# Kernel tuning notes

Measured on AMD Instinct MI355X. Metric: run time of the kernel, lower is better.

## Reference

```python
import jax, jax.numpy as jnp
import numpy as np

B, S, D = 8, 1024, 1024
N_HEAD, N_ACTIVE, D_ATTN = 16, 4, 128

def setup_inputs() -> dict:
    key = jax.random.key(0)
    ks = jax.random.split(key, 8)
    sc = 0.02
    return {
        "x": jax.random.normal(ks[0], (B, S, D), jnp.float32),
        "Wq": jax.random.normal(ks[1], (N_HEAD, D, D_ATTN), jnp.float32) * sc,
        "bq": jnp.zeros((N_HEAD, D_ATTN), jnp.float32),
        "Wk": jax.random.normal(ks[2], (N_HEAD, D, D_ATTN), jnp.float32) * sc,
        "bk": jnp.zeros((N_HEAD, D_ATTN), jnp.float32),
        "Wv": jax.random.normal(ks[3], (N_HEAD, D, D_ATTN), jnp.float32) * sc,
        "bv": jnp.zeros((N_HEAD, D_ATTN), jnp.float32),
        "Wr": jax.random.normal(ks[4], (D, N_HEAD), jnp.float32) * sc,
        "br": jnp.zeros((N_HEAD,), jnp.float32),
        "Wo": jax.random.normal(ks[5], (N_ACTIVE * D_ATTN, D), jnp.float32) * sc,
        "bo": jnp.zeros((D,), jnp.float32),
    }

def reference(x, Wq, bq, Wk, bk, Wv, bv, Wr, br, Wo, bo):
    # ---- routing: mean-pool router logits over seq, softmax over heads ----
    logits = jnp.einsum('bsd,dh->bsh', x, Wr) + br          # [B,S,H]
    dist = jax.nn.softmax(logits.mean(axis=1), axis=-1)     # [B,H]
    vals, idx = jax.lax.top_k(dist, N_ACTIVE)               # [B,A]
    # zeros + scatter of top-k probs, then softmax over ALL heads (as in source)
    sparse = jnp.zeros_like(dist).at[jnp.arange(B)[:, None], idx].set(vals)
    gates_full = jax.nn.softmax(sparse, axis=-1)            # [B,H]
    gates = jnp.take_along_axis(gates_full, idx, axis=-1)   # [B,A]
    # ---- gather active-head projection weights per batch ----
    Wq_a, Wk_a, Wv_a = Wq[idx], Wk[idx], Wv[idx]            # [B,A,D,Dk]
    bq_a, bk_a, bv_a = bq[idx], bk[idx], bv[idx]            # [B,A,Dk]
    Q = jnp.einsum('bsd,badk->bask', x, Wq_a) + bq_a[:, :, None, :]
    K = jnp.einsum('bsd,badk->bask', x, Wk_a) + bk_a[:, :, None, :]
    V = jnp.einsum('bsd,badk->bask', x, Wv_a) + bv_a[:, :, None, :]
    scale = 1.0 / jnp.sqrt(jnp.asarray(D_ATTN, x.dtype))
    scores = jax.nn.softmax(jnp.einsum('bask,batk->bast', Q, K) * scale, axis=-1)
    heads = jnp.einsum('bast,batk->bask', scores, V)        # [B,A,S,Dk]
    heads = heads * gates[:, :, None, None]                 # gate each head
    # concat active heads -> [B,S,A*Dk], output projection
    cat = heads.transpose(0, 2, 1, 3).reshape(B, S, N_ACTIVE * D_ATTN)
    return jnp.einsum('bsf,fd->bsd', cat, Wo) + bo
```

## Files before the change

### kernel.cpp

```cpp
#include <hip/hip_runtime.h>
#include <math.h>

#define NB 8
#define SQ 1024
#define DM 1024
#define NH 16
#define NA 4
#define DKH 128

#define WS_XPART 0
#define WS_IDX   524288
#define WS_GATES 524416
#define WS_XB    524800
#define WS_WQT   (WS_XB  + 16777216)
#define WS_WKT   (WS_WQT + 4194304)
#define WS_WVT   (WS_WKT + 4194304)
#define WS_WOT   (WS_WVT + 4194304)
#define WS_Q     (WS_WOT + 1048576)
#define WS_K     (WS_Q  + 8388608)
#define WS_VT    (WS_K  + 8388608)
#define WS_CAT   (WS_VT + 8388608)

typedef __attribute__((ext_vector_type(8))) short short8;
typedef __attribute__((ext_vector_type(4))) short short4v;
typedef __attribute__((ext_vector_type(4))) float f32x4;

#define MFMA16(a, b, c) __builtin_amdgcn_mfma_f32_16x16x32_bf16(a, b, c, 0, 0, 0)
#define GLL16(g, l) __builtin_amdgcn_global_load_lds( \
    (const __attribute__((address_space(1))) void*)(g), \
    (__attribute__((address_space(3))) void*)(l), 16, 0, 0)

__device__ __forceinline__ short f2bf(float f) {
  unsigned u = __float_as_uint(f);
  u += 0x7FFF + ((u >> 16) & 1);
  return (short)(u >> 16);
}

__global__ __launch_bounds__(256) void k_prep(const float* __restrict__ x,
                                              short* __restrict__ xb,
                                              float* __restrict__ xpart) {
  int b = blockIdx.x, ch = blockIdx.y;
  const float* xp = x + ((size_t)b*SQ + (size_t)ch*64)*DM;
  short* xbp = xb + ((size_t)b*SQ + (size_t)ch*64)*DM;
  int t = threadIdx.x;
  float a0 = 0.f, a1 = 0.f, a2 = 0.f, a3 = 0.f;
  #pragma unroll 4
  for (int r = 0; r < 64; r++) {
    float4 v = *(const float4*)&xp[(size_t)r*DM + t*4];
    short4v s4;
    s4[0] = f2bf(v.x); s4[1] = f2bf(v.y); s4[2] = f2bf(v.z); s4[3] = f2bf(v.w);
    *(short4v*)&xbp[(size_t)r*DM + t*4] = s4;
    a0 += v.x; a1 += v.y; a2 += v.z; a3 += v.w;
  }
  float4 o = {a0, a1, a2, a3};
  *(float4*)&xpart[((size_t)b*16 + ch)*DM + t*4] = o;
}

__device__ __forceinline__ void tc_tile(const float* __restrict__ in,
                                        short* __restrict__ outb,
                                        int R, int C, int r0, int c0,
                                        float (*t)[33]) {
  int tx = threadIdx.x, ty = threadIdx.y;
  #pragma unroll
  for (int i = 0; i < 4; i++)
    t[ty + 8*i][tx] = in[(size_t)(r0 + ty + 8*i) * C + c0 + tx];
  __syncthreads();
  #pragma unroll
  for (int i = 0; i < 4; i++)
    outb[(size_t)(c0 + ty + 8*i) * R + r0 + tx] = f2bf(t[tx][ty + 8*i]);
}

__global__ __launch_bounds__(256) void k_tw(
    const float* __restrict__ Wq, const float* __restrict__ Wk,
    const float* __restrict__ Wv, const float* __restrict__ Wo,
    short* __restrict__ Wqt, short* __restrict__ Wkt,
    short* __restrict__ Wvt, short* __restrict__ Wot) {
  __shared__ float t[32][33];
  int blk = blockIdx.x;
  if (blk < 6144) {
    int zz = blk >> 7;
    int within = blk & 127;
    int m = zz >> 4, hh = zz & 15;
    const float* in = (m == 0 ? Wq : m == 1 ? Wk : Wv) + (size_t)hh * DM * DKH;
    short* outb = (m == 0 ? Wqt : m == 1 ? Wkt : Wvt) + (size_t)hh * DM * DKH;
    int r0 = (within & 31) * 32;
    int c0 = (within >> 5) * 32;
    tc_tile(in, outb, DM, DKH, r0, c0, t);
  } else {
    int w2 = blk - 6144;
    int r0 = (w2 & 15) * 32;
    int c0 = (w2 >> 4) * 32;
    tc_tile(Wo, Wot, NA*DKH, DM, r0, c0, t);
  }
}

__global__ __launch_bounds__(256) void k_router(const float* __restrict__ xpart,
                                                const float* __restrict__ Wr,
                                                const float* __restrict__ br,
                                                int* __restrict__ idxout,
                                                float* __restrict__ gatesout) {
  __shared__ float xm[DM];
  __shared__ float red[16][17];
  __shared__ float logits[NH];
  int b = blockIdx.x;
  int t = threadIdx.x;
  #pragma unroll
  for (int i = 0; i < 4; i++) {
    int d = t + 256*i;
    float s = 0.f;
    for (int c = 0; c < 16; c++) s += xpart[((size_t)b*16 + c)*DM + d];
    xm[d] = s * (1.0f/(float)SQ);
  }
  __syncthreads();
  {
    int h = t & 15, c16 = t >> 4;
    float p = 0.f;
    #pragma unroll 8
    for (int j = 0; j < 64; j++) {
      int d = c16*64 + j;
      p += xm[d] * Wr[(size_t)d*NH + h];
    }
    red[c16][h] = p;
  }
  __syncthreads();
  if (t < NH) {
    float lg = br[t];
    #pragma unroll
    for (int c = 0; c < 16; c++) lg += red[c][t];
    logits[t] = lg;
  }
  __syncthreads();
  if (t == 0) {
    float mx = logits[0];
    for (int h = 1; h < NH; h++) mx = fmaxf(mx, logits[h]);
    float e[NH], sum = 0.f;
    for (int h = 0; h < NH; h++) { e[h] = expf(logits[h]-mx); sum += e[h]; }
    float dist[NH];
    for (int h = 0; h < NH; h++) dist[h] = e[h]/sum;
    int idx[NA]; float vals[NA]; bool used[NH];
    for (int h = 0; h < NH; h++) used[h] = false;
    for (int a = 0; a < NA; a++) {
      int best = -1; float bv = -1.f;
      for (int h = 0; h < NH; h++)
        if (!used[h] && dist[h] > bv) { bv = dist[h]; best = h; }
      used[best] = true; idx[a] = best; vals[a] = bv;
    }
    float sp[NH];
    for (int h = 0; h < NH; h++) sp[h] = 0.f;
    for (int a = 0; a < NA; a++) sp[idx[a]] = vals[a];
    float m2 = sp[0];
    for (int h = 1; h < NH; h++) m2 = fmaxf(m2, sp[h]);
    float e2[NH], s2 = 0.f;
    for (int h = 0; h < NH; h++) { e2[h] = expf(sp[h]-m2); s2 += e2[h]; }
    for (int a = 0; a < NA; a++) {
      idxout[b*NA + a]   = idx[a];
      gatesout[b*NA + a] = e2[idx[a]] / s2;
    }
  }
}

__global__ __launch_bounds__(512, 2) void k_qkv(
    const short* __restrict__ xb, const short* __restrict__ Wqt,
    const short* __restrict__ Wkt, const short* __restrict__ Wvt,
    const float* __restrict__ bq, const float* __restrict__ bk,
    const float* __restrict__ bv, const int* __restrict__ idxb,
    short* __restrict__ Qo, short* __restrict__ Ko, short* __restrict__ Vto) {
  __shared__ __align__(16) short As[2][128*64];
  __shared__ __align__(16) short Bs[2][384*64];
  int blk = blockIdx.x;
  int b = blk & 7;
  int rest = blk >> 3;
  int a4 = rest & 3;
  int mt = rest >> 2;
  int z = b*NA + a4;
  int h = idxb[z];
  const short* Ag = xb + (size_t)b*SQ*DM + (size_t)mt*128*DM;
  int tid = threadIdx.x, lane = tid & 63, wid = tid >> 6;
  int wm = wid & 1, wn = wid >> 1;
  int l15 = lane & 15, quad = lane >> 4, l7 = lane & 7, srow = lane >> 3;
  int scol = (l7 ^ srow) * 8;
  const short* Wp;
  {
    int whichw = (wid - 2) >> 1;
    const short* Wbase = (whichw == 0) ? Wqt : (whichw == 1) ? Wkt : Wvt;
    Wp = Wbase + (size_t)h * (DKH * DM);
  }
  int brow_base = ((wid - 2) & 1) * 64;

#define STAGE_QKV(KT, AS, BS) do {                                          \
    if (wid < 2) {                                                          \
      _Pragma("unroll")                                                     \
      for (int i_ = 0; i_ < 8; i_++) {                                      \
        int slot_ = wid*8 + i_;                                             \
        GLL16(Ag + (size_t)(slot_*8 + srow)*DM + (KT)*64 + scol,            \
              (AS) + slot_*512);                                            \
      }                                                                     \
    } else {                                                                \
      _Pragma("unroll")                                                     \
      for (int i_ = 0; i_ < 8; i_++) {                                      \
        int bslot_ = (wid-2)*8 + i_;                                        \
        GLL16(Wp + (size_t)(brow_base + i_*8 + srow)*DM + (KT)*64 + scol,   \
              (BS) + bslot_*512);                                           \
      }                                                                     \
    }                                                                       \
  } while (0)

  f32x4 acc[4][6];
  #pragma unroll
  for (int i = 0; i < 4; i++)
    #pragma unroll
    for (int j = 0; j < 6; j++) acc[i][j] = (f32x4){0.f,0.f,0.f,0.f};

  STAGE_QKV(0, &As[0][0], &Bs[0][0]);

  for (int kt = 0; kt < 16; kt++) {
    int cur = kt & 1;
    asm volatile("s_waitcnt vmcnt(0)" ::: "memory");
    __syncthreads();
    if (kt + 1 < 16)
      STAGE_QKV(kt + 1, &As[cur ^ 1][0], &Bs[cur ^ 1][0]);
    #pragma unroll
    for (int ks = 0; ks < 2; ks++) {
      int kc = ks*4 + quad;
      short8 a[4], bf[6];
      #pragma unroll
      for (int mi = 0; mi < 4; mi++)
        a[mi] = *(const short8*)&As[cur][(wm*64 + mi*16 + l15)*64 + ((kc ^ l7)*8)];
      #pragma unroll
      for (int ni = 0; ni < 6; ni++)
        bf[ni] = *(const short8*)&Bs[cur][(wn*96 + ni*16 + l15)*64 + ((kc ^ l7)*8)];
      #pragma unroll
      for (int mi = 0; mi < 4; mi++)
        #pragma unroll
        for (int ni = 0; ni < 6; ni++)
          acc[mi][ni] = MFMA16(a[mi], bf[ni], acc[mi][ni]);
    }
  }
#undef STAGE_QKV

  #pragma unroll
  for (int ni = 0; ni < 6; ni++) {
    int col = wn*96 + ni*16 + l15;
    int whichc = (wn*96 + ni*16) >> 7;
    int cl = col & 127;
    const float* bp = (whichc == 0) ? bq : (whichc == 1) ? bk : bv;
    float bcol = bp[h*DKH + cl];
    if (whichc < 2) {
      short* outp = ((whichc == 0) ? Qo : Ko) + (size_t)z*SQ*DKH;
      #pragma unroll
      for (int mi = 0; mi < 4; mi++) {
        #pragma unroll
        for (int r = 0; r < 4; r++) {
          int row = mt*128 + wm*64 + mi*16 + quad*4 + r;
          outp[(size_t)row*DKH + cl] = f2bf(acc[mi][ni][r] + bcol);
        }
      }
    } else {
      short* outp = Vto + (size_t)z*DKH*SQ;
      #pragma unroll
      for (int mi = 0; mi < 4; mi++) {
        int row0 = mt*128 + wm*64 + mi*16 + quad*4;
        short4v v;
        #pragma unroll
        for (int r = 0; r < 4; r++) v[r] = f2bf(acc[mi][ni][r] + bcol);
        *(short4v*)&outp[(size_t)cl*SQ + row0] = v;
      }
    }
  }
}

__global__ __launch_bounds__(256) void k_attn(
    const short* __restrict__ Qg, const short* __restrict__ Kg,
    const short* __restrict__ Vtg, const float* __restrict__ gates,
    short* __restrict__ cat) {
  __shared__ __align__(16) short Ks[2][64*128];
  __shared__ __align__(16) short Vts[2][128*64];
  __shared__ __align__(16) short Ps[4*16*72];
  int blk = blockIdx.x;
  int slot = blk >> 3;
  int z = (blk & 7) + 8*(slot & 3);
  int qt = slot >> 2;
  int b = z >> 2, hs = z & 3;
  int tid = threadIdx.x, lane = tid & 63, wid = tid >> 6;
  int l15 = lane & 15, quad = lane >> 4, l7 = lane & 7, lby8 = lane >> 3;
  const short* Qp = Qg + ((size_t)z*SQ + (size_t)qt*64)*DKH;
  const short* Kp = Kg + (size_t)z*SQ*DKH;
  const short* Vp = Vtg + (size_t)z*DKH*SQ;
  short8 qa[4];
  #pragma unroll
  for (int ks = 0; ks < 4; ks++)
    qa[ks] = *(const short8*)&Qp[(size_t)(wid*16 + l15)*DKH + (ks*4 + quad)*8];
  #pragma unroll
  for (int i = 0; i < 4; i++) {
    int ci = wid*4 + i;
    int r = ci*4 + quad;
    int sc = ((l15 ^ (r & 15)) * 8);
    GLL16(Kp + (size_t)r*DKH + sc, &Ks[0][ci*512]);
    int rv = ci*8 + lby8;
    int scv = ((l7 ^ lby8) * 8);
    GLL16(Vp + (size_t)rv*SQ + scv, &Vts[0][ci*512]);
  }
  f32x4 O[8];
  #pragma unroll
  for (int dn = 0; dn < 8; dn++) O[dn] = (f32x4){0.f,0.f,0.f,0.f};
  float lsum[4] = {0.f, 0.f, 0.f, 0.f};
  const float scale = 0.08838834764831845f;
  for (int t = 0; t < 16; t++) {
    int cur = t & 1;
    asm volatile("s_waitcnt vmcnt(0)" ::: "memory");
    __syncthreads();
    if (t + 1 < 16) {
      #pragma unroll
      for (int i = 0; i < 4; i++) {
        int ci = wid*4 + i;
        int r = ci*4 + quad;
        int sc = ((l15 ^ (r & 15)) * 8);
        GLL16(Kp + (size_t)((t+1)*64 + r)*DKH + sc, &Ks[cur^1][ci*512]);
        int rv = ci*8 + lby8;
        int scv = ((l7 ^ lby8) * 8);
        GLL16(Vp + (size_t)rv*SQ + (t+1)*64 + scv, &Vts[cur^1][ci*512]);
      }
    }
    f32x4 s[4];
    #pragma unroll
    for (int nj = 0; nj < 4; nj++) s[nj] = (f32x4){0.f,0.f,0.f,0.f};
    #pragma unroll
    for (int ks = 0; ks < 4; ks++) {
      int kc = ks*4 + quad;
      #pragma unroll
      for (int nj = 0; nj < 4; nj++) {
        short8 bk8 = *(const short8*)&Ks[cur][(nj*16 + l15)*128 + ((kc ^ l15)*8)];
        s[nj] = MFMA16(qa[ks], bk8, s[nj]);
      }
    }
    #pragma unroll
    for (int r = 0; r < 4; r++) {
      float p0 = __expf(s[0][r]*scale);
      float p1 = __expf(s[1][r]*scale);
      float p2 = __expf(s[2][r]*scale);
      float p3 = __expf(s[3][r]*scale);
      lsum[r] += p0 + p1 + p2 + p3;
      int pbase = wid*1152 + (quad*4 + r)*72;
      Ps[pbase +  0 + l15] = f2bf(p0);
      Ps[pbase + 16 + l15] = f2bf(p1);
      Ps[pbase + 32 + l15] = f2bf(p2);
      Ps[pbase + 48 + l15] = f2bf(p3);
    }
    asm volatile("s_waitcnt lgkmcnt(0)" ::: "memory");
    #pragma unroll
    for (int ks2 = 0; ks2 < 2; ks2++) {
      int kc = ks2*4 + quad;
      short8 pa = *(const short8*)&Ps[wid*1152 + l15*72 + kc*8];
      #pragma unroll
      for (int dn = 0; dn < 8; dn++) {
        short8 bv8 = *(const short8*)&Vts[cur][(dn*16 + l15)*64 + ((kc ^ l7)*8)];
        O[dn] = MFMA16(pa, bv8, O[dn]);
      }
    }
  }
  float gate = gates[z];
  #pragma unroll
  for (int r = 0; r < 4; r++) {
    float rs = lsum[r];
    rs += __shfl_xor(rs, 1); rs += __shfl_xor(rs, 2);
    rs += __shfl_xor(rs, 4); rs += __shfl_xor(rs, 8);
    float sc2 = gate / rs;
    int row = qt*64 + wid*16 + quad*4 + r;
    short* cp = cat + ((size_t)(b*SQ + row))*(NA*DKH) + hs*DKH;
    #pragma unroll
    for (int dn = 0; dn < 8; dn++)
      cp[dn*16 + l15] = f2bf(O[dn][r] * sc2);
  }
}

__global__ __launch_bounds__(256) void k_out(
    const short* __restrict__ catb, const short* __restrict__ Wot,
    const float* __restrict__ bo, float* __restrict__ out) {
  __shared__ __align__(16) short As[2][128*64];
  __shared__ __align__(16) short Bs[2][128*64];
  int blk = blockIdx.x;
  int mt = (blk & 7) + 8*(blk >> 6);
  int nt = (blk >> 3) & 7;
  const short* Ag = catb + (size_t)mt*128*(NA*DKH);
  const short* Bg = Wot + (size_t)nt*128*(NA*DKH);
  int tid = threadIdx.x, lane = tid & 63, wid = tid >> 6;
  int wm = wid & 1, wn = wid >> 1;
  int l15 = lane & 15, quad = lane >> 4, l7 = lane & 7, lby8 = lane >> 3;
  int srow = lby8;
  int scol = ((l7 ^ lby8) * 8);
  f32x4 acc[4][4];
  #pragma unroll
  for (int i = 0; i < 4; i++)
    #pragma unroll
    for (int j = 0; j < 4; j++) acc[i][j] = (f32x4){0.f,0.f,0.f,0.f};
  #pragma unroll
  for (int i = 0; i < 4; i++) {
    int ci = wid*4 + i;
    GLL16(Ag + (size_t)(ci*8 + srow)*(NA*DKH) + scol, &As[0][ci*512]);
    GLL16(Bg + (size_t)(ci*8 + srow)*(NA*DKH) + scol, &Bs[0][ci*512]);
  }
  for (int kt = 0; kt < 8; kt++) {
    int cur = kt & 1;
    asm volatile("s_waitcnt vmcnt(0)" ::: "memory");
    __syncthreads();
    if (kt + 1 < 8) {
      #pragma unroll
      for (int i = 0; i < 4; i++) {
        int ci = wid*4 + i;
        GLL16(Ag + (size_t)(ci*8 + srow)*(NA*DKH) + (kt+1)*64 + scol, &As[cur^1][ci*512]);
        GLL16(Bg + (size_t)(ci*8 + srow)*(NA*DKH) + (kt+1)*64 + scol, &Bs[cur^1][ci*512]);
      }
    }
    #pragma unroll
    for (int ks = 0; ks < 2; ks++) {
      int kc = ks*4 + quad;
      short8 a[4], bf[4];
      #pragma unroll
      for (int mi = 0; mi < 4; mi++)
        a[mi] = *(const short8*)&As[cur][(wm*64 + mi*16 + l15)*64 + ((kc ^ l7)*8)];
      #pragma unroll
      for (int ni = 0; ni < 4; ni++)
        bf[ni] = *(const short8*)&Bs[cur][(wn*64 + ni*16 + l15)*64 + ((kc ^ l7)*8)];
      #pragma unroll
      for (int mi = 0; mi < 4; mi++)
        #pragma unroll
        for (int ni = 0; ni < 4; ni++)
          acc[mi][ni] = MFMA16(a[mi], bf[ni], acc[mi][ni]);
    }
  }
  #pragma unroll
  for (int mi = 0; mi < 4; mi++)
    #pragma unroll
    for (int ni = 0; ni < 4; ni++) {
      int col = nt*128 + wn*64 + ni*16 + l15;
      float bcol = bo[col];
      #pragma unroll
      for (int r = 0; r < 4; r++) {
        int row = mt*128 + wm*64 + mi*16 + quad*4 + r;
        out[(size_t)row*DM + col] = acc[mi][ni][r] + bcol;
      }
    }
}

extern "C" void kernel_launch(void* const* d_in, const int* in_sizes, int n_in,
                              void* d_out, int out_size, void* d_ws, size_t ws_size,
                              hipStream_t stream) {
  const float* x  = (const float*)d_in[0];
  const float* Wq = (const float*)d_in[1];
  const float* bq = (const float*)d_in[2];
  const float* Wk = (const float*)d_in[3];
  const float* bk = (const float*)d_in[4];
  const float* Wv = (const float*)d_in[5];
  const float* bv = (const float*)d_in[6];
  const float* Wr = (const float*)d_in[7];
  const float* br = (const float*)d_in[8];
  const float* Wo = (const float*)d_in[9];
  const float* bo = (const float*)d_in[10];
  char* ws = (char*)d_ws;
  float* xpart = (float*)(ws + WS_XPART);
  int*   idxb  = (int*)(ws + WS_IDX);
  float* gat   = (float*)(ws + WS_GATES);
  short* xb    = (short*)(ws + WS_XB);
  short* Wqt   = (short*)(ws + WS_WQT);
  short* Wkt   = (short*)(ws + WS_WKT);
  short* Wvt   = (short*)(ws + WS_WVT);
  short* Wot   = (short*)(ws + WS_WOT);
  short* Qb    = (short*)(ws + WS_Q);
  short* Kb    = (short*)(ws + WS_K);
  short* Vtb   = (short*)(ws + WS_VT);
  short* catb  = (short*)(ws + WS_CAT);
  float* out   = (float*)d_out;

  k_prep<<<dim3(NB,16), 256, 0, stream>>>(x, xb, xpart);
  k_router<<<NB, 256, 0, stream>>>(xpart, Wr, br, idxb, gat);
  k_tw<<<6656, dim3(32,8), 0, stream>>>(Wq, Wk, Wv, Wo, Wqt, Wkt, Wvt, Wot);
  k_qkv<<<256, 512, 0, stream>>>(xb, Wqt, Wkt, Wvt, bq, bk, bv, idxb, Qb, Kb, Vtb);
  k_attn<<<512, 256, 0, stream>>>(Qb, Kb, Vtb, gat, catb);
  k_out<<<512, 256, 0, stream>>>(catb, Wot, bo, out);
}
```

Before: 218.4 us.

## Merge prep and weight-transpose kernels; deepen GEMM pipelines to 4-stage K=32

Folds the x bf16-conversion/partial-sum kernel into the weight-transpose kernel, giving one launch with a flat grid. The QKV and output GEMMs move from 2-stage double buffering with 64-wide K tiles to 4-stage ring buffers with 32-wide K tiles and a new swizzle. Three stages are prefetched ahead and the loop uses partial vmcnt waits, so loads overlap MFMA work instead of draining every iteration. This costs twice as many barriers and K iterations, and relies on the hand-counted vmcnt values being correct.

```diff
diff --git a/kernel.cpp b/kernel.cpp
--- a/kernel.cpp
+++ b/kernel.cpp
@@ -36,31 +36,15 @@
   return (short)(u >> 16);
 }
 
-__global__ __launch_bounds__(256) void k_prep(const float* __restrict__ x,
-                                              short* __restrict__ xb,
-                                              float* __restrict__ xpart) {
-  int b = blockIdx.x, ch = blockIdx.y;
-  const float* xp = x + ((size_t)b*SQ + (size_t)ch*64)*DM;
-  short* xbp = xb + ((size_t)b*SQ + (size_t)ch*64)*DM;
-  int t = threadIdx.x;
-  float a0 = 0.f, a1 = 0.f, a2 = 0.f, a3 = 0.f;
-  #pragma unroll 4
-  for (int r = 0; r < 64; r++) {
-    float4 v = *(const float4*)&xp[(size_t)r*DM + t*4];
-    short4v s4;
-    s4[0] = f2bf(v.x); s4[1] = f2bf(v.y); s4[2] = f2bf(v.z); s4[3] = f2bf(v.w);
-    *(short4v*)&xbp[(size_t)r*DM + t*4] = s4;
-    a0 += v.x; a1 += v.y; a2 += v.z; a3 += v.w;
-  }
-  float4 o = {a0, a1, a2, a3};
-  *(float4*)&xpart[((size_t)b*16 + ch)*DM + t*4] = o;
+__device__ __forceinline__ int swz32(int r, int q) {
+  int g = ((r & 1) << 2) | q;
+  return ((r >> 1) << 6) + ((g ^ ((r >> 1) & 7)) << 3);
 }
 
 __device__ __forceinline__ void tc_tile(const float* __restrict__ in,
                                         short* __restrict__ outb,
                                         int R, int C, int r0, int c0,
-                                        float (*t)[33]) {
-  int tx = threadIdx.x, ty = threadIdx.y;
+                                        float (*t)[33], int tx, int ty) {
   #pragma unroll
   for (int i = 0; i < 4; i++)
     t[ty + 8*i][tx] = in[(size_t)(r0 + ty + 8*i) * C + c0 + tx];
@@ -70,27 +54,49 @@
     outb[(size_t)(c0 + ty + 8*i) * R + r0 + tx] = f2bf(t[tx][ty + 8*i]);
 }
 
-__global__ __launch_bounds__(256) void k_tw(
+__global__ __launch_bounds__(256) void k_pt(
+    const float* __restrict__ x, short* __restrict__ xb,
+    float* __restrict__ xpart,
     const float* __restrict__ Wq, const float* __restrict__ Wk,
     const float* __restrict__ Wv, const float* __restrict__ Wo,
     short* __restrict__ Wqt, short* __restrict__ Wkt,
     short* __restrict__ Wvt, short* __restrict__ Wot) {
   __shared__ float t[32][33];
   int blk = blockIdx.x;
-  if (blk < 6144) {
-    int zz = blk >> 7;
-    int within = blk & 127;
-    int m = zz >> 4, hh = zz & 15;
-    const float* in = (m == 0 ? Wq : m == 1 ? Wk : Wv) + (size_t)hh * DM * DKH;
-    short* outb = (m == 0 ? Wqt : m == 1 ? Wkt : Wvt) + (size_t)hh * DM * DKH;
-    int r0 = (within & 31) * 32;
-    int c0 = (within >> 5) * 32;
-    tc_tile(in, outb, DM, DKH, r0, c0, t);
+  if (blk < 128) {
+    int b = blk >> 4, ch = blk & 15;
+    const float* xp = x + ((size_t)b*SQ + (size_t)ch*64)*DM;
+    short* xbp = xb + ((size_t)b*SQ + (size_t)ch*64)*DM;
+    int tt = threadIdx.x;
+    float a0 = 0.f, a1 = 0.f, a2 = 0.f, a3 = 0.f;
+    #pragma unroll 4
+    for (int r = 0; r < 64; r++) {
+      float4 v = *(const float4*)&xp[(size_t)r*DM + tt*4];
+      short4v s4;
+      s4[0] = f2bf(v.x); s4[1] = f2bf(v.y); s4[2] = f2bf(v.z); s4[3] = f2bf(v.w);
+      *(short4v*)&xbp[(size_t)r*DM + tt*4] = s4;
+      a0 += v.x; a1 += v.y; a2 += v.z; a3 += v.w;
+    }
+    float4 o = {a0, a1, a2, a3};
+    *(float4*)&xpart[((size_t)b*16 + ch)*DM + tt*4] = o;
   } else {
-    int w2 = blk - 6144;
-    int r0 = (w2 & 15) * 32;
-    int c0 = (w2 >> 4) * 32;
-    tc_tile(Wo, Wot, NA*DKH, DM, r0, c0, t);
+    int tb = blk - 128;
+    int tx = threadIdx.x & 31, ty = threadIdx.x >> 5;
+    if (tb < 6144) {
+      int zz = tb >> 7;
+      int within = tb & 127;
+      int m = zz >> 4, hh = zz & 15;
+      const float* in = (m == 0 ? Wq : m == 1 ? Wk : Wv) + (size_t)hh * DM * DKH;
+      short* outb = (m == 0 ? Wqt : m == 1 ? Wkt : Wvt) + (size_t)hh * DM * DKH;
+      int r0 = (within & 31) * 32;
+      int c0 = (within >> 5) * 32;
+      tc_tile(in, outb, DM, DKH, r0, c0, t, tx, ty);
+    } else {
+      int w2 = tb - 6144;
+      int r0 = (w2 & 15) * 32;
+      int c0 = (w2 >> 4) * 32;
+      tc_tile(Wo, Wot, NA*DKH, DM, r0, c0, t, tx, ty);
+    }
   }
 }
 
@@ -165,8 +171,8 @@
     const float* __restrict__ bq, const float* __restrict__ bk,
     const float* __restrict__ bv, const int* __restrict__ idxb,
     short* __restrict__ Qo, short* __restrict__ Ko, short* __restrict__ Vto) {
-  __shared__ __align__(16) short As[2][128*64];
-  __shared__ __align__(16) short Bs[2][384*64];
+  __shared__ __align__(16) short As[4][128*32];
+  __shared__ __align__(16) short Bs[4][384*32];
   int blk = blockIdx.x;
   int b = blk & 7;
   int rest = blk >> 3;
@@ -177,30 +183,32 @@
   const short* Ag = xb + (size_t)b*SQ*DM + (size_t)mt*128*DM;
   int tid = threadIdx.x, lane = tid & 63, wid = tid >> 6;
   int wm = wid & 1, wn = wid >> 1;
-  int l15 = lane & 15, quad = lane >> 4, l7 = lane & 7, srow = lane >> 3;
-  int scol = (l7 ^ srow) * 8;
+  int l15 = lane & 15, quad = lane >> 4;
+  int rr8 = lane >> 3;
+  int gl  = (lane & 7) ^ rr8;
+  int rin = rr8*2 + (gl >> 2);
+  int kq8 = (gl & 3) * 8;
   const short* Wp;
   {
     int whichw = (wid - 2) >> 1;
     const short* Wbase = (whichw == 0) ? Wqt : (whichw == 1) ? Wkt : Wvt;
     Wp = Wbase + (size_t)h * (DKH * DM);
   }
-  int brow_base = ((wid - 2) & 1) * 64;
-
-#define STAGE_QKV(KT, AS, BS) do {                                          \
+  int brow = ((wid - 2) & 1) * 64;
+
+#define STAGE_Q(T) do {                                                     \
+    int bi_ = (T) & 3; int kb_ = (T)*32;                                    \
     if (wid < 2) {                                                          \
       _Pragma("unroll")                                                     \
-      for (int i_ = 0; i_ < 8; i_++) {                                      \
-        int slot_ = wid*8 + i_;                                             \
-        GLL16(Ag + (size_t)(slot_*8 + srow)*DM + (KT)*64 + scol,            \
-              (AS) + slot_*512);                                            \
+      for (int i_ = 0; i_ < 4; i_++) {                                      \
+        int s_ = wid*4 + i_;                                                \
+        GLL16(Ag + (size_t)(s_*16 + rin)*DM + kb_ + kq8, &As[bi_][s_*512]); \
       }                                                                     \
     } else {                                                                \
       _Pragma("unroll")                                                     \
-      for (int i_ = 0; i_ < 8; i_++) {                                      \
-        int bslot_ = (wid-2)*8 + i_;                                        \
-        GLL16(Wp + (size_t)(brow_base + i_*8 + srow)*DM + (KT)*64 + scol,   \
-              (BS) + bslot_*512);                                           \
+      for (int i_ = 0; i_ < 4; i_++) {                                      \
+        GLL16(Wp + (size_t)(brow + i_*16 + rin)*DM + kb_ + kq8,             \
+              &Bs[bi_][((wid-2)*4 + i_)*512]);                              \
       }                                                                     \
     }                                                                       \
   } while (0)
@@ -211,32 +219,29 @@
     #pragma unroll
     for (int j = 0; j < 6; j++) acc[i][j] = (f32x4){0.f,0.f,0.f,0.f};
 
-  STAGE_QKV(0, &As[0][0], &Bs[0][0]);
-
-  for (int kt = 0; kt < 16; kt++) {
-    int cur = kt & 1;
-    asm volatile("s_waitcnt vmcnt(0)" ::: "memory");
+  STAGE_Q(0); STAGE_Q(1); STAGE_Q(2);
+
+  for (int kt = 0; kt < 32; kt++) {
+    int buf = kt & 3;
+    if (kt < 30)       asm volatile("s_waitcnt vmcnt(8)" ::: "memory");
+    else if (kt == 30) asm volatile("s_waitcnt vmcnt(4)" ::: "memory");
+    else               asm volatile("s_waitcnt vmcnt(0)" ::: "memory");
     __syncthreads();
-    if (kt + 1 < 16)
-      STAGE_QKV(kt + 1, &As[cur ^ 1][0], &Bs[cur ^ 1][0]);
-    #pragma unroll
-    for (int ks = 0; ks < 2; ks++) {
-      int kc = ks*4 + quad;
-      short8 a[4], bf[6];
-      #pragma unroll
-      for (int mi = 0; mi < 4; mi++)
-        a[mi] = *(const short8*)&As[cur][(wm*64 + mi*16 + l15)*64 + ((kc ^ l7)*8)];
+    if (kt + 3 < 32) STAGE_Q(kt + 3);
+    short8 a[4], bf[6];
+    #pragma unroll
+    for (int mi = 0; mi < 4; mi++)
+      a[mi] = *(const short8*)&As[buf][swz32(wm*64 + mi*16 + l15, quad)];
+    #pragma unroll
+    for (int ni = 0; ni < 6; ni++)
+      bf[ni] = *(const short8*)&Bs[buf][swz32(wn*96 + ni*16 + l15, quad)];
+    #pragma unroll
+    for (int mi = 0; mi < 4; mi++)
       #pragma unroll
       for (int ni = 0; ni < 6; ni++)
-        bf[ni] = *(const short8*)&Bs[cur][(wn*96 + ni*16 + l15)*64 + ((kc ^ l7)*8)];
-      #pragma unroll
-      for (int mi = 0; mi < 4; mi++)
-        #pragma unroll
-        for (int ni = 0; ni < 6; ni++)
-          acc[mi][ni] = MFMA16(a[mi], bf[ni], acc[mi][ni]);
-    }
-  }
-#undef STAGE_QKV
+        acc[mi][ni] = MFMA16(a[mi], bf[ni], acc[mi][ni]);
+  }
+#undef STAGE_Q
 
   #pragma unroll
   for (int ni = 0; ni < 6; ni++) {
@@ -376,8 +381,8 @@
 __global__ __launch_bounds__(256) void k_out(
     const short* __restrict__ catb, const short* __restrict__ Wot,
     const float* __restrict__ bo, float* __restrict__ out) {
-  __shared__ __align__(16) short As[2][128*64];
-  __shared__ __align__(16) short Bs[2][128*64];
+  __shared__ __align__(16) short As[4][128*32];
+  __shared__ __align__(16) short Bs[4][128*32];
   int blk = blockIdx.x;
   int mt = (blk & 7) + 8*(blk >> 6);
   int nt = (blk >> 3) & 7;
@@ -385,49 +390,61 @@
   const short* Bg = Wot + (size_t)nt*128*(NA*DKH);
   int tid = threadIdx.x, lane = tid & 63, wid = tid >> 6;
   int wm = wid & 1, wn = wid >> 1;
-  int l15 = lane & 15, quad = lane >> 4, l7 = lane & 7, lby8 = lane >> 3;
-  int srow = lby8;
-  int scol = ((l7 ^ lby8) * 8);
+  int l15 = lane & 15, quad = lane >> 4;
+  int rr8 = lane >> 3;
+  int gl  = (lane & 7) ^ rr8;
+  int rin = rr8*2 + (gl >> 2);
+  int kq8 = (gl & 3) * 8;
+
+#define STAGE_O(T) do {                                                       \
+    int bi_ = (T) & 3; int kb_ = (T)*32;                                      \
+    if (wid < 2) {                                                            \
+      _Pragma("unroll")                                                       \
+      for (int i_ = 0; i_ < 4; i_++) {                                        \
+        int s_ = wid*4 + i_;                                                  \
+        GLL16(Ag + (size_t)(s_*16 + rin)*(NA*DKH) + kb_ + kq8,                \
+              &As[bi_][s_*512]);                                              \
+      }                                                                       \
+    } else {                                                                  \
+      _Pragma("unroll")                                                       \
+      for (int i_ = 0; i_ < 4; i_++) {                                        \
+        int s_ = (wid-2)*4 + i_;                                              \
+        GLL16(Bg + (size_t)(s_*16 + rin)*(NA*DKH) + kb_ + kq8,                \
+              &Bs[bi_][s_*512]);                                              \
+      }                                                                       \
+    }                                                                         \
+  } while (0)
+
   f32x4 acc[4][4];
   #pragma unroll
   for (int i = 0; i < 4; i++)
     #pragma unroll
     for (int j = 0; j < 4; j++) acc[i][j] = (f32x4){0.f,0.f,0.f,0.f};
-  #pragma unroll
-  for (int i = 0; i < 4; i++) {
-    int ci = wid*4 + i;
-    GLL16(Ag + (size_t)(ci*8 + srow)*(NA*DKH) + scol, &As[0][ci*512]);
-    GLL16(Bg + (size_t)(ci*8 + srow)*(NA*DKH) + scol, &Bs[0][ci*512]);
-  }
-  for (int kt = 0; kt < 8; kt++) {
-    int cur = kt & 1;
-    asm volatile("s_waitcnt vmcnt(0)" ::: "memory");
+
+  STAGE_O(0); STAGE_O(1); STAGE_O(2);
+
+  for (int kt = 0; kt < 16; kt++) {
+    int buf = kt & 3;
+    if (kt < 14)       asm volatile("s_waitcnt vmcnt(8)" ::: "memory");
+    else if (kt == 14) asm volatile("s_waitcnt vmcnt(4)" ::: "memory");
+    else               asm volatile("s_waitcnt vmcnt(0)" ::: "memory");
     __syncthreads();
-    if (kt + 1 < 8) {
-      #pragma unroll
-      for (int i = 0; i < 4; i++) {
-        int ci = wid*4 + i;
-        GLL16(Ag + (size_t)(ci*8 + srow)*(NA*DKH) + (kt+1)*64 + scol, &As[cur^1][ci*512]);
-        GLL16(Bg + (size_t)(ci*8 + srow)*(NA*DKH) + (kt+1)*64 + scol, &Bs[cur^1][ci*512]);
-      }
-    }
-    #pragma unroll
-    for (int ks = 0; ks < 2; ks++) {
-      int kc = ks*4 + quad;
-      short8 a[4], bf[4];
-      #pragma unroll
-      for (int mi = 0; mi < 4; mi++)
-        a[mi] = *(const short8*)&As[cur][(wm*64 + mi*16 + l15)*64 + ((kc ^ l7)*8)];
+    if (kt + 3 < 16) STAGE_O(kt + 3);
+    short8 a[4], bf[4];
+    #pragma unroll
+    for (int mi = 0; mi < 4; mi++)
+      a[mi] = *(const short8*)&As[buf][swz32(wm*64 + mi*16 + l15, quad)];
+    #pragma unroll
+    for (int ni = 0; ni < 4; ni++)
+      bf[ni] = *(const short8*)&Bs[buf][swz32(wn*64 + ni*16 + l15, quad)];
+    #pragma unroll
+    for (int mi = 0; mi < 4; mi++)
       #pragma unroll
       for (int ni = 0; ni < 4; ni++)
-        bf[ni] = *(const short8*)&Bs[cur][(wn*64 + ni*16 + l15)*64 + ((kc ^ l7)*8)];
-      #pragma unroll
-      for (int mi = 0; mi < 4; mi++)
-        #pragma unroll
-        for (int ni = 0; ni < 4; ni++)
-          acc[mi][ni] = MFMA16(a[mi], bf[ni], acc[mi][ni]);
-    }
-  }
+        acc[mi][ni] = MFMA16(a[mi], bf[ni], acc[mi][ni]);
+  }
+#undef STAGE_O
+
   #pragma unroll
   for (int mi = 0; mi < 4; mi++)
     #pragma unroll
@@ -471,9 +488,8 @@
   short* catb  = (short*)(ws + WS_CAT);
   float* out   = (float*)d_out;
 
-  k_prep<<<dim3(NB,16), 256, 0, stream>>>(x, xb, xpart);
+  k_pt<<<6784, 256, 0, stream>>>(x, xb, xpart, Wq, Wk, Wv, Wo, Wqt, Wkt, Wvt, Wot);
   k_router<<<NB, 256, 0, stream>>>(xpart, Wr, br, idxb, gat);
-  k_tw<<<6656, dim3(32,8), 0, stream>>>(Wq, Wk, Wv, Wo, Wqt, Wkt, Wvt, Wot);
   k_qkv<<<256, 512, 0, stream>>>(xb, Wqt, Wkt, Wvt, bq, bk, bv, idxb, Qb, Kb, Vtb);
   k_attn<<<512, 256, 0, stream>>>(Qb, Kb, Vtb, gat, catb);
   k_out<<<512, 256, 0, stream>>>(catb, Wot, bo, out);
```

New measurement: 226.1 us. +3.5%, slower.

## Merge prep and weight-transpose kernels; split K/V prefetch in attention with priorities

Applied to the files above, without the earlier changes.

The x bf16 conversion/partial-sum kernel and the weight transpose kernel are merged into one launch, which removes a launch and lets the two independent jobs run at the same time. In the attention loop, the K and V tile prefetches are now issued separately. V is loaded after the QK^T and softmax phase, with partial vmcnt waits so that K and V loads overlap different compute phases. s_setprio raises wave priority around the MFMA sections. The cost is an extra __syncthreads per iteration and more delicate wait-count bookkeeping.

```diff
diff --git a/kernel.cpp b/kernel.cpp
--- a/kernel.cpp
+++ b/kernel.cpp
@@ -36,31 +36,10 @@
   return (short)(u >> 16);
 }
 
-__global__ __launch_bounds__(256) void k_prep(const float* __restrict__ x,
-                                              short* __restrict__ xb,
-                                              float* __restrict__ xpart) {
-  int b = blockIdx.x, ch = blockIdx.y;
-  const float* xp = x + ((size_t)b*SQ + (size_t)ch*64)*DM;
-  short* xbp = xb + ((size_t)b*SQ + (size_t)ch*64)*DM;
-  int t = threadIdx.x;
-  float a0 = 0.f, a1 = 0.f, a2 = 0.f, a3 = 0.f;
-  #pragma unroll 4
-  for (int r = 0; r < 64; r++) {
-    float4 v = *(const float4*)&xp[(size_t)r*DM + t*4];
-    short4v s4;
-    s4[0] = f2bf(v.x); s4[1] = f2bf(v.y); s4[2] = f2bf(v.z); s4[3] = f2bf(v.w);
-    *(short4v*)&xbp[(size_t)r*DM + t*4] = s4;
-    a0 += v.x; a1 += v.y; a2 += v.z; a3 += v.w;
-  }
-  float4 o = {a0, a1, a2, a3};
-  *(float4*)&xpart[((size_t)b*16 + ch)*DM + t*4] = o;
-}
-
 __device__ __forceinline__ void tc_tile(const float* __restrict__ in,
                                         short* __restrict__ outb,
                                         int R, int C, int r0, int c0,
-                                        float (*t)[33]) {
-  int tx = threadIdx.x, ty = threadIdx.y;
+                                        float (*t)[33], int tx, int ty) {
   #pragma unroll
   for (int i = 0; i < 4; i++)
     t[ty + 8*i][tx] = in[(size_t)(r0 + ty + 8*i) * C + c0 + tx];
@@ -70,27 +49,49 @@
     outb[(size_t)(c0 + ty + 8*i) * R + r0 + tx] = f2bf(t[tx][ty + 8*i]);
 }
 
-__global__ __launch_bounds__(256) void k_tw(
+__global__ __launch_bounds__(256) void k_pt(
+    const float* __restrict__ x, short* __restrict__ xb,
+    float* __restrict__ xpart,
     const float* __restrict__ Wq, const float* __restrict__ Wk,
     const float* __restrict__ Wv, const float* __restrict__ Wo,
     short* __restrict__ Wqt, short* __restrict__ Wkt,
     short* __restrict__ Wvt, short* __restrict__ Wot) {
   __shared__ float t[32][33];
   int blk = blockIdx.x;
-  if (blk < 6144) {
-    int zz = blk >> 7;
-    int within = blk & 127;
-    int m = zz >> 4, hh = zz & 15;
-    const float* in = (m == 0 ? Wq : m == 1 ? Wk : Wv) + (size_t)hh * DM * DKH;
-    short* outb = (m == 0 ? Wqt : m == 1 ? Wkt : Wvt) + (size_t)hh * DM * DKH;
-    int r0 = (within & 31) * 32;
-    int c0 = (within >> 5) * 32;
-    tc_tile(in, outb, DM, DKH, r0, c0, t);
+  if (blk < 128) {
+    int b = blk >> 4, ch = blk & 15;
+    const float* xp = x + ((size_t)b*SQ + (size_t)ch*64)*DM;
+    short* xbp = xb + ((size_t)b*SQ + (size_t)ch*64)*DM;
+    int tt = threadIdx.x;
+    float a0 = 0.f, a1 = 0.f, a2 = 0.f, a3 = 0.f;
+    #pragma unroll 4
+    for (int r = 0; r < 64; r++) {
+      float4 v = *(const float4*)&xp[(size_t)r*DM + tt*4];
+      short4v s4;
+      s4[0] = f2bf(v.x); s4[1] = f2bf(v.y); s4[2] = f2bf(v.z); s4[3] = f2bf(v.w);
+      *(short4v*)&xbp[(size_t)r*DM + tt*4] = s4;
+      a0 += v.x; a1 += v.y; a2 += v.z; a3 += v.w;
+    }
+    float4 o = {a0, a1, a2, a3};
+    *(float4*)&xpart[((size_t)b*16 + ch)*DM + tt*4] = o;
   } else {
-    int w2 = blk - 6144;
-    int r0 = (w2 & 15) * 32;
-    int c0 = (w2 >> 4) * 32;
-    tc_tile(Wo, Wot, NA*DKH, DM, r0, c0, t);
+    int tb = blk - 128;
+    int tx = threadIdx.x & 31, ty = threadIdx.x >> 5;
+    if (tb < 6144) {
+      int zz = tb >> 7;
+      int within = tb & 127;
+      int m = zz >> 4, hh = zz & 15;
+      const float* in = (m == 0 ? Wq : m == 1 ? Wk : Wv) + (size_t)hh * DM * DKH;
+      short* outb = (m == 0 ? Wqt : m == 1 ? Wkt : Wvt) + (size_t)hh * DM * DKH;
+      int r0 = (within & 31) * 32;
+      int c0 = (within >> 5) * 32;
+      tc_tile(in, outb, DM, DKH, r0, c0, t, tx, ty);
+    } else {
+      int w2 = tb - 6144;
+      int r0 = (w2 & 15) * 32;
+      int c0 = (w2 >> 4) * 32;
+      tc_tile(Wo, Wot, NA*DKH, DM, r0, c0, t, tx, ty);
+    }
   }
 }
 
@@ -296,6 +297,10 @@
     int r = ci*4 + quad;
     int sc = ((l15 ^ (r & 15)) * 8);
     GLL16(Kp + (size_t)r*DKH + sc, &Ks[0][ci*512]);
+  }
+  #pragma unroll
+  for (int i = 0; i < 4; i++) {
+    int ci = wid*4 + i;
     int rv = ci*8 + lby8;
     int scv = ((l7 ^ lby8) * 8);
     GLL16(Vp + (size_t)rv*SQ + scv, &Vts[0][ci*512]);
@@ -307,7 +312,7 @@
   const float scale = 0.08838834764831845f;
   for (int t = 0; t < 16; t++) {
     int cur = t & 1;
-    asm volatile("s_waitcnt vmcnt(0)" ::: "memory");
+    asm volatile("s_waitcnt vmcnt(4)" ::: "memory");
     __syncthreads();
     if (t + 1 < 16) {
       #pragma unroll
@@ -316,14 +321,12 @@
         int r = ci*4 + quad;
         int sc = ((l15 ^ (r & 15)) * 8);
         GLL16(Kp + (size_t)((t+1)*64 + r)*DKH + sc, &Ks[cur^1][ci*512]);
-        int rv = ci*8 + lby8;
-        int scv = ((l7 ^ lby8) * 8);
-        GLL16(Vp + (size_t)rv*SQ + (t+1)*64 + scv, &Vts[cur^1][ci*512]);
       }
     }
     f32x4 s[4];
     #pragma unroll
     for (int nj = 0; nj < 4; nj++) s[nj] = (f32x4){0.f,0.f,0.f,0.f};
+    __builtin_amdgcn_s_setprio(1);
     #pragma unroll
     for (int ks = 0; ks < 4; ks++) {
       int kc = ks*4 + quad;
@@ -333,6 +336,7 @@
         s[nj] = MFMA16(qa[ks], bk8, s[nj]);
       }
     }
+    __builtin_amdgcn_s_setprio(0);
     #pragma unroll
     for (int r = 0; r < 4; r++) {
       float p0 = __expf(s[0][r]*scale);
@@ -346,7 +350,20 @@
       Ps[pbase + 32 + l15] = f2bf(p2);
       Ps[pbase + 48 + l15] = f2bf(p3);
     }
+    if (t + 1 < 16) asm volatile("s_waitcnt vmcnt(4)" ::: "memory");
+    else            asm volatile("s_waitcnt vmcnt(0)" ::: "memory");
+    __syncthreads();
+    if (t + 1 < 16) {
+      #pragma unroll
+      for (int i = 0; i < 4; i++) {
+        int ci = wid*4 + i;
+        int rv = ci*8 + lby8;
+        int scv = ((l7 ^ lby8) * 8);
+        GLL16(Vp + (size_t)rv*SQ + (t+1)*64 + scv, &Vts[cur^1][ci*512]);
+      }
+    }
     asm volatile("s_waitcnt lgkmcnt(0)" ::: "memory");
+    __builtin_amdgcn_s_setprio(1);
     #pragma unroll
     for (int ks2 = 0; ks2 < 2; ks2++) {
       int kc = ks2*4 + quad;
@@ -357,6 +374,7 @@
         O[dn] = MFMA16(pa, bv8, O[dn]);
       }
     }
+    __builtin_amdgcn_s_setprio(0);
   }
   float gate = gates[z];
   #pragma unroll
@@ -471,9 +489,8 @@
   short* catb  = (short*)(ws + WS_CAT);
   float* out   = (float*)d_out;
 
-  k_prep<<<dim3(NB,16), 256, 0, stream>>>(x, xb, xpart);
+  k_pt<<<6784, 256, 0, stream>>>(x, xb, xpart, Wq, Wk, Wv, Wo, Wqt, Wkt, Wvt, Wot);
   k_router<<<NB, 256, 0, stream>>>(xpart, Wr, br, idxb, gat);
-  k_tw<<<6656, dim3(32,8), 0, stream>>>(Wq, Wk, Wv, Wo, Wqt, Wkt, Wvt, Wot);
   k_qkv<<<256, 512, 0, stream>>>(xb, Wqt, Wkt, Wvt, bq, bk, bv, idxb, Qb, Kb, Vtb);
   k_attn<<<512, 256, 0, stream>>>(Qb, Kb, Vtb, gat, catb);
   k_out<<<512, 256, 0, stream>>>(catb, Wot, bo, out);
```

Result: no change. 217.2 us (-0.6%).
